# Optimization experiments

Measured on AMD Instinct MI355X. Metric: run time of the kernel, lower is better.

## Reference

```python
import jax, jax.numpy as jnp
import numpy as np

D = 1024
H = 16
T_BLOCK = 2048


def setup_inputs() -> dict:
    key = jax.random.key(0)
    ks = jax.random.split(key, 12)
    B, T = 2, 2048
    s = lambda k, shape: jax.random.normal(k, shape, jnp.float32) * 0.02
    return {
        "x": jax.random.normal(ks[0], (B, T, D), jnp.float32),
        # layernorms
        "ln1_g": jnp.ones((D,), jnp.float32), "ln1_b": jnp.zeros((D,), jnp.float32),
        "ln2_g": jnp.ones((D,), jnp.float32), "ln2_b": jnp.zeros((D,), jnp.float32),
        # attention qkv projection ([in,out] layout) and output proj
        "w_qkv": s(ks[1], (D, 3 * D)), "b_qkv": jnp.zeros((3 * D,), jnp.float32),
        "w_o": s(ks[2], (D, D)), "b_o": jnp.zeros((D,), jnp.float32),
        # MLP
        "w_fc1": s(ks[3], (D, 4 * D)), "b_fc1": jnp.zeros((4 * D,), jnp.float32),
        "w_fc2": s(ks[4], (4 * D, D)), "b_fc2": jnp.zeros((D,), jnp.float32),
    }


def _layernorm(x, g, b, eps=1e-5):
    mu = jnp.mean(x, axis=-1, keepdims=True)
    var = jnp.var(x, axis=-1, keepdims=True)
    return (x - mu) * jax.lax.rsqrt(var + eps) * g + b


def _attention(x, w_qkv, b_qkv, w_o, b_o):
    B, T, C = x.shape
    hd = C // H
    qkv = x @ w_qkv + b_qkv                      # [B,T,3C]
    q, k, v = jnp.split(qkv, 3, axis=-1)
    split = lambda t: t.reshape(B, T, H, hd).transpose(0, 2, 1, 3)  # [B,H,T,hd]
    q, k, v = split(q), split(k), split(v)
    att = jnp.einsum("bhqd,bhkd->bhqk", q, k) / jnp.sqrt(jnp.float32(hd))
    causal = jnp.tril(jnp.ones((T, T), bool))
    att = jnp.where(causal[None, None], att, -jnp.inf)
    att = jax.nn.softmax(att, axis=-1)
    y = jnp.einsum("bhqk,bhkd->bhqd", att, v)    # [B,H,T,hd]
    y = y.transpose(0, 2, 1, 3).reshape(B, T, C)
    return y @ w_o + b_o


def reference(x, ln1_g, ln1_b, ln2_g, ln2_b, w_qkv, b_qkv, w_o, b_o,
              w_fc1, b_fc1, w_fc2, b_fc2):
    # dropout is identity in eval mode
    x = x + _attention(_layernorm(x, ln1_g, ln1_b), w_qkv, b_qkv, w_o, b_o)
    h = jax.nn.gelu(_layernorm(x, ln2_g, ln2_b) @ w_fc1 + b_fc1)
    return x + (h @ w_fc2 + b_fc2)
```

## Files before the change

### kernel.cpp

```cpp
#include <hip/hip_runtime.h>
#include <hip/hip_bf16.h>


using bf16 = __bf16;
using bf16x8 = __attribute__((ext_vector_type(8))) __bf16;
using floatx4 = __attribute__((ext_vector_type(4))) float;

#define D_ 1024
#define T_ 2048
#define B_ 2
#define H_ 16

static __device__ __forceinline__ bf16 f2bf(float f) { return (bf16)f; }

static __device__ __forceinline__ void async16(const void* g, void* l) {
  __builtin_amdgcn_global_load_lds(
      (const __attribute__((address_space(1))) void*)g,
      (__attribute__((address_space(3))) void*)l, 16, 0, 0);
}

static __device__ __forceinline__ float gelu_f(float v) {
  const float u2 = 1.5957691216057308f * (v + 0.044715f * v * v * v);
  return v / (1.0f + __expf(-u2));
}

__global__ void transpose_cast(const float* __restrict__ in, bf16* __restrict__ out,
                               int K, int N) {
  __shared__ float tile[32][33];
  const int n0 = blockIdx.x * 32, k0 = blockIdx.y * 32;
  const int tx = threadIdx.x, ty = threadIdx.y;
  for (int i = 0; i < 32; i += 8)
    tile[ty + i][tx] = in[(size_t)(k0 + ty + i) * N + n0 + tx];
  __syncthreads();
  for (int i = 0; i < 32; i += 8)
    out[(size_t)(n0 + ty + i) * K + k0 + tx] = f2bf(tile[tx][ty + i]);
}

__global__ __launch_bounds__(256)
void ln_kernel(const float* __restrict__ x, const float* __restrict__ g,
               const float* __restrict__ bsh, bf16* __restrict__ out) {
  const int row = blockIdx.x, tid = threadIdx.x;
  const float4 v = ((const float4*)(x + (size_t)row * D_))[tid];
  float s = v.x + v.y + v.z + v.w;
  float s2 = v.x * v.x + v.y * v.y + v.z * v.z + v.w * v.w;
  for (int off = 32; off; off >>= 1) {
    s += __shfl_xor(s, off);
    s2 += __shfl_xor(s2, off);
  }
  __shared__ float red[8];
  const int wave = tid >> 6, lane = tid & 63;
  if (lane == 0) { red[wave] = s; red[wave + 4] = s2; }
  __syncthreads();
  s = red[0] + red[1] + red[2] + red[3];
  s2 = red[4] + red[5] + red[6] + red[7];
  const float mu = s * (1.0f / D_);
  const float rstd = rsqrtf(s2 * (1.0f / D_) - mu * mu + 1e-5f);
  const float4 gv = ((const float4*)g)[tid];
  const float4 bv = ((const float4*)bsh)[tid];
  bf16 o[4] __attribute__((aligned(8)));
  o[0] = f2bf((v.x - mu) * rstd * gv.x + bv.x);
  o[1] = f2bf((v.y - mu) * rstd * gv.y + bv.y);
  o[2] = f2bf((v.z - mu) * rstd * gv.z + bv.z);
  o[3] = f2bf((v.w - mu) * rstd * gv.w + bv.w);
  *(ushort4*)(out + (size_t)row * D_ + tid * 4) = *(const ushort4*)o;
}

template <int EPI>
__global__ __launch_bounds__(256)
void gemm_bt(const bf16* __restrict__ A, const bf16* __restrict__ Bt,
             const float* __restrict__ bias, const float* __restrict__ res,
             void* __restrict__ Cout, int M, int N, int K) {
  __shared__ __align__(16) bf16 As[128][64];
  __shared__ __align__(16) bf16 Bs[128][64];
  const int tid = threadIdx.x;
  const int wave = tid >> 6, lane = tid & 63;
  const int quad = lane >> 4, l16 = lane & 15;
  const int wr = wave >> 1, wc = wave & 1;
  const int bm = blockIdx.x * 128, bn = blockIdx.y * 128;
  const int lrow8 = lane >> 3;
  const int lcol = (((lane & 7) ^ lrow8) * 8);

  floatx4 acc[4][4] = {};

  for (int k0 = 0; k0 < K; k0 += 64) {
    __syncthreads();
    for (int c = 0; c < 4; c++) {
      const int r = wave * 32 + c * 8;
      async16(&A[(size_t)(bm + r + lrow8) * K + k0 + lcol], &As[r][0]);
      async16(&Bt[(size_t)(bn + r + lrow8) * K + k0 + lcol], &Bs[r][0]);
    }
    __syncthreads();
    for (int ks = 0; ks < 2; ks++) {
      const int fc = ((quad + ks * 4) ^ (l16 & 7)) * 8;
      bf16x8 af[4], bfr[4];
      for (int mt = 0; mt < 4; mt++)
        af[mt] = *(const bf16x8*)&As[wr * 64 + mt * 16 + l16][fc];
      for (int nt = 0; nt < 4; nt++)
        bfr[nt] = *(const bf16x8*)&Bs[wc * 64 + nt * 16 + l16][fc];
      for (int mt = 0; mt < 4; mt++)
        for (int nt = 0; nt < 4; nt++)
          acc[mt][nt] = __builtin_amdgcn_mfma_f32_16x16x32_bf16(
              af[mt], bfr[nt], acc[mt][nt], 0, 0, 0);
    }
  }

  for (int mt = 0; mt < 4; mt++) {
    for (int nt = 0; nt < 4; nt++) {
      const int col = bn + wc * 64 + nt * 16 + l16;
      const float bcol = bias[col];
      for (int i = 0; i < 4; i++) {
        const int row = bm + wr * 64 + mt * 16 + quad * 4 + i;
        float v = acc[mt][nt][i] + bcol;
        if (EPI == 0) {
          ((bf16*)Cout)[(size_t)row * N + col] = f2bf(v);
        } else if (EPI == 1) {
          ((bf16*)Cout)[(size_t)row * N + col] = f2bf(gelu_f(v));
        } else {
          ((float*)Cout)[(size_t)row * N + col] = v + res[(size_t)row * N + col];
        }
      }
    }
  }
}

template <int EPI>
__global__ __launch_bounds__(256)
void gemm64_k128(const bf16* __restrict__ A, const bf16* __restrict__ Bt,
                 const float* __restrict__ bias, const float* __restrict__ res,
                 void* __restrict__ Cout, int M, int N, int K) {
  __shared__ __align__(16) bf16 As[64][128];
  __shared__ __align__(16) bf16 Bs[128][128];
  const int tid = threadIdx.x;
  const int wave = tid >> 6, lane = tid & 63;
  const int quad = lane >> 4, l16 = lane & 15;
  const int wr = wave >> 1, wc = wave & 1;
  const int bm = blockIdx.x * 64, bn = blockIdx.y * 128;
  const int sr = lane >> 4;
  const int pchunk = lane & 15;

  floatx4 acc[2][4] = {};

  for (int k0 = 0; k0 < K; k0 += 128) {
    __syncthreads();
    for (int c = 0; c < 4; c++) {
      const int base = wave * 16 + c * 4;
      const int scol = (pchunk ^ ((c * 4 + sr) & 15)) * 8;
      async16(&A[(size_t)(bm + base + sr) * K + k0 + scol], &As[base][0]);
    }
    for (int c = 0; c < 8; c++) {
      const int base = wave * 32 + c * 4;
      const int scol = (pchunk ^ ((c * 4 + sr) & 15)) * 8;
      async16(&Bt[(size_t)(bn + base + sr) * K + k0 + scol], &Bs[base][0]);
    }
    __syncthreads();
    for (int ks = 0; ks < 4; ks++) {
      const int fc = ((quad + ks * 4) ^ l16) * 8;
      bf16x8 af[2], bfr[4];
      for (int mt = 0; mt < 2; mt++)
        af[mt] = *(const bf16x8*)&As[wr * 32 + mt * 16 + l16][fc];
      for (int nt = 0; nt < 4; nt++)
        bfr[nt] = *(const bf16x8*)&Bs[wc * 64 + nt * 16 + l16][fc];
      for (int mt = 0; mt < 2; mt++)
        for (int nt = 0; nt < 4; nt++)
          acc[mt][nt] = __builtin_amdgcn_mfma_f32_16x16x32_bf16(
              af[mt], bfr[nt], acc[mt][nt], 0, 0, 0);
    }
  }

  for (int mt = 0; mt < 2; mt++) {
    for (int nt = 0; nt < 4; nt++) {
      const int col = bn + wc * 64 + nt * 16 + l16;
      const float bcol = bias[col];
      for (int i = 0; i < 4; i++) {
        const int row = bm + wr * 32 + mt * 16 + quad * 4 + i;
        float v = acc[mt][nt][i] + bcol;
        if (EPI == 0) {
          ((bf16*)Cout)[(size_t)row * N + col] = f2bf(v);
        } else if (EPI == 1) {
          ((bf16*)Cout)[(size_t)row * N + col] = f2bf(gelu_f(v));
        } else {
          ((float*)Cout)[(size_t)row * N + col] = v + res[(size_t)row * N + col];
        }
      }
    }
  }
}

__global__ __launch_bounds__(512)
void attn_kernel(const bf16* __restrict__ qkv, bf16* __restrict__ y) {
  const int bh = blockIdx.y, b = bh >> 4, h = bh & 15;
  const int tile = (blockIdx.y & 16) ? (int)blockIdx.x : (15 - (int)blockIdx.x);
  const int q0 = tile * 128;
  const int tid = threadIdx.x, wave = tid >> 6, lane = tid & 63;
  const int quad = lane >> 4, l16 = lane & 15;
  const int l7 = l16 & 7;
  const int w16 = wave * 16;

  __shared__ __align__(16) bf16 Ks[64][64];
  __shared__ __align__(16) bf16 Vts[64][64];
  __shared__ __align__(16) bf16 Ps[128][64];

  const size_t bbase = (size_t)b * T_ * 3072 + (size_t)h * 64;
  const bf16* Qg = qkv + bbase;
  const bf16* Kg = qkv + bbase + 1024;
  const bf16* Vg = qkv + bbase + 2048;

  bf16x8 ones;
  for (int j = 0; j < 8; j++) ones[j] = f2bf(1.0f);

  const int kr = tid >> 3, kch = tid & 7;
  const int kcol = ((kch ^ (kr & 7)) * 8);
  const int vk = tid & 63, vd = tid >> 6;

  bf16x8 qf[2];
  for (int ks = 0; ks < 2; ks++) {
    bf16x8 t = *(const bf16x8*)
        &Qg[(size_t)(q0 + w16 + l16) * 3072 + ks * 32 + quad * 8];
    for (int j = 0; j < 8; j++) t[j] = f2bf((float)t[j] * 0.125f);
    qf[ks] = t;
  }

  int4 kreg = *(const int4*)&Kg[(size_t)kr * 3072 + kch * 8];
  bf16x8 vreg = *(const bf16x8*)&Vg[(size_t)vk * 3072 + vd * 8];

  floatx4 accY[4] = {};
  floatx4 accL = {};

  const int kend = q0 + 64;
  for (int kc = 0; kc <= kend; kc += 64) {
    __syncthreads();
    *(int4*)&Ks[kr][kcol] = kreg;
    for (int j = 0; j < 8; j++) {
      const int d = vd * 8 + j;
      Vts[d][((vk >> 3) ^ j) * 8 + (vk & 7)] = vreg[j];
    }
    __syncthreads();

    if (kc < kend) {
      kreg = *(const int4*)&Kg[(size_t)(kc + 64 + kr) * 3072 + kch * 8];
      vreg = *(const bf16x8*)&Vg[(size_t)(kc + 64 + vk) * 3072 + vd * 8];
    }

    floatx4 s[4];
    for (int nt = 0; nt < 4; nt++) {
      const bf16* krow = &Ks[nt * 16 + l16][0];
      bf16x8 kf0 = *(const bf16x8*)&krow[(quad ^ l7) * 8];
      bf16x8 kf1 = *(const bf16x8*)&krow[((4 + quad) ^ l7) * 8];
      floatx4 t = {};
      t = __builtin_amdgcn_mfma_f32_16x16x32_bf16(qf[0], kf0, t, 0, 0, 0);
      t = __builtin_amdgcn_mfma_f32_16x16x32_bf16(qf[1], kf1, t, 0, 0, 0);
      s[nt] = t;
    }
    if (kc + 64 > q0 + w16) {
      for (int nt = 0; nt < 4; nt++)
        for (int i = 0; i < 4; i++) {
          const int c = kc + nt * 16 + l16;
          const int r = q0 + w16 + quad * 4 + i;
          if (c > r) s[nt][i] = -1e30f;
        }
    }

    for (int i = 0; i < 4; i++) {
      const int pr = quad * 4 + i;
      bf16* prow = &Ps[w16 + pr][0];
      for (int nt = 0; nt < 4; nt++)
        prow[(((nt * 2 + (l16 >> 3)) ^ (pr & 7)) * 8) + l7] =
            f2bf(__expf(s[nt][i] - 8.0f));
    }
    __builtin_amdgcn_wave_barrier();

    for (int ks = 0; ks < 2; ks++) {
      bf16x8 pa = *(const bf16x8*)&Ps[w16 + l16][((ks * 4 + quad) ^ l7) * 8];
      for (int dt = 0; dt < 4; dt++) {
        bf16x8 vb = *(const bf16x8*)&Vts[dt * 16 + l16][((ks * 4 + quad) ^ l7) * 8];
        accY[dt] =
            __builtin_amdgcn_mfma_f32_16x16x32_bf16(pa, vb, accY[dt], 0, 0, 0);
      }
      accL = __builtin_amdgcn_mfma_f32_16x16x32_bf16(pa, ones, accL, 0, 0, 0);
    }
  }

  for (int i = 0; i < 4; i++) {
    const float linv = 1.0f / accL[i];
    const int r = q0 + w16 + quad * 4 + i;
    for (int dt = 0; dt < 4; dt++)
      y[(size_t)(b * T_ + r) * D_ + h * 64 + dt * 16 + l16] =
          f2bf(accY[dt][i] * linv);
  }
}

extern "C" void kernel_launch(void* const* d_in, const int* in_sizes, int n_in,
                              void* d_out, int out_size, void* d_ws, size_t ws_size,
                              hipStream_t stream) {
  const float* x     = (const float*)d_in[0];
  const float* ln1_g = (const float*)d_in[1];
  const float* ln1_b = (const float*)d_in[2];
  const float* ln2_g = (const float*)d_in[3];
  const float* ln2_b = (const float*)d_in[4];
  const float* w_qkv = (const float*)d_in[5];
  const float* b_qkv = (const float*)d_in[6];
  const float* w_o   = (const float*)d_in[7];
  const float* b_o   = (const float*)d_in[8];
  const float* w_fc1 = (const float*)d_in[9];
  const float* b_fc1 = (const float*)d_in[10];
  const float* w_fc2 = (const float*)d_in[11];
  const float* b_fc2 = (const float*)d_in[12];

  char* p = (char*)d_ws;
  bf16* wqkvT = (bf16*)p; p += (size_t)3072 * 1024 * 2;
  bf16* woT   = (bf16*)p; p += (size_t)1024 * 1024 * 2;
  bf16* wfc1T = (bf16*)p; p += (size_t)4096 * 1024 * 2;
  bf16* wfc2T = (bf16*)p; p += (size_t)1024 * 4096 * 2;
  bf16* ln1   = (bf16*)p; p += (size_t)4096 * 1024 * 2;
  bf16* qkv   = (bf16*)p; p += (size_t)4096 * 3072 * 2;
  bf16* yb    = (bf16*)p; p += (size_t)4096 * 1024 * 2;
  float* x2   = (float*)p; p += (size_t)4096 * 1024 * 4;
  bf16* ln2   = (bf16*)p; p += (size_t)4096 * 1024 * 2;
  bf16* hb    = (bf16*)p; p += (size_t)4096 * 4096 * 2;

  const dim3 tb(32, 8);
  transpose_cast<<<dim3(96, 32), tb, 0, stream>>>(w_qkv, wqkvT, 1024, 3072);
  transpose_cast<<<dim3(32, 32), tb, 0, stream>>>(w_o, woT, 1024, 1024);
  transpose_cast<<<dim3(128, 32), tb, 0, stream>>>(w_fc1, wfc1T, 1024, 4096);
  transpose_cast<<<dim3(32, 128), tb, 0, stream>>>(w_fc2, wfc2T, 4096, 1024);

  ln_kernel<<<4096, 256, 0, stream>>>(x, ln1_g, ln1_b, ln1);
  gemm_bt<0><<<dim3(32, 24), 256, 0, stream>>>(ln1, wqkvT, b_qkv, nullptr, qkv,
                                               4096, 3072, 1024);
  attn_kernel<<<dim3(16, 32), 512, 0, stream>>>(qkv, yb);
  gemm64_k128<2><<<dim3(64, 8), 256, 0, stream>>>(yb, woT, b_o, x, x2,
                                                  4096, 1024, 1024);
  ln_kernel<<<4096, 256, 0, stream>>>(x2, ln2_g, ln2_b, ln2);
  gemm_bt<1><<<dim3(32, 32), 256, 0, stream>>>(ln2, wfc1T, b_fc1, nullptr, hb,
                                               4096, 4096, 1024);
  gemm64_k128<2><<<dim3(64, 8), 256, 0, stream>>>(hb, wfc2T, b_fc2, x2, (float*)d_out,
                                                  4096, 1024, 4096);
}
```

Baseline: 319.0 us.

## Double-buffer LDS tiles in gemm_bt with async prefetch two steps ahead

Converts the 128x128 GEMM main loop to a two-stage LDS ping-pong. The global-to-LDS loads for step t+2 are issued while step t computes, and a partial vmcnt wait lets in-flight loads overlap MFMA work. This removes the full load-then-compute serialization of each K step, at the cost of doubling LDS use to 64KB per block, which may lower occupancy.

Measured after the change: 319.1 us. No clear change (+0.0%).

```diff
diff --git a/kernel.cpp b/kernel.cpp
--- a/kernel.cpp
+++ b/kernel.cpp
@@ -70,8 +70,8 @@
 void gemm_bt(const bf16* __restrict__ A, const bf16* __restrict__ Bt,
              const float* __restrict__ bias, const float* __restrict__ res,
              void* __restrict__ Cout, int M, int N, int K) {
-  __shared__ __align__(16) bf16 As[128][64];
-  __shared__ __align__(16) bf16 Bs[128][64];
+  __shared__ __align__(16) bf16 As[2][128][64];
+  __shared__ __align__(16) bf16 Bs[2][128][64];
   const int tid = threadIdx.x;
   const int wave = tid >> 6, lane = tid & 63;
   const int quad = lane >> 4, l16 = lane & 15;
@@ -80,37 +80,55 @@
   const int lrow8 = lane >> 3;
   const int lcol = (((lane & 7) ^ lrow8) * 8);
 
+  const bf16* aBase = &A[(size_t)(bm + wave * 32 + lrow8) * K + lcol];
+  const bf16* bBase = &Bt[(size_t)(bn + wave * 32 + lrow8) * K + lcol];
+
+  auto stage = [&](int buf, int kk) {
+    const int k0 = kk * 64;
+    for (int c = 0; c < 4; c++) {
+      async16(aBase + (size_t)c * 8 * K + k0, &As[buf][wave * 32 + c * 8][0]);
+      async16(bBase + (size_t)c * 8 * K + k0, &Bs[buf][wave * 32 + c * 8][0]);
+    }
+  };
+
   floatx4 acc[4][4] = {};
-
-  for (int k0 = 0; k0 < K; k0 += 64) {
-    __syncthreads();
-    for (int c = 0; c < 4; c++) {
-      const int r = wave * 32 + c * 8;
-      async16(&A[(size_t)(bm + r + lrow8) * K + k0 + lcol], &As[r][0]);
-      async16(&Bt[(size_t)(bn + r + lrow8) * K + k0 + lcol], &Bs[r][0]);
-    }
-    __syncthreads();
+  const int nsteps = K >> 6;
+
+  stage(0, 0);
+  if (nsteps > 1) stage(1, 1);
+  int cur = 0;
+  for (int t = 0; t < nsteps; ++t) {
+    if (t < nsteps - 1)
+      asm volatile("s_waitcnt vmcnt(8)" ::: "memory");
+    else
+      asm volatile("s_waitcnt vmcnt(0)" ::: "memory");
+    __builtin_amdgcn_s_barrier();
+    __builtin_amdgcn_sched_barrier(0);
     for (int ks = 0; ks < 2; ks++) {
       const int fc = ((quad + ks * 4) ^ (l16 & 7)) * 8;
       bf16x8 af[4], bfr[4];
       for (int mt = 0; mt < 4; mt++)
-        af[mt] = *(const bf16x8*)&As[wr * 64 + mt * 16 + l16][fc];
-      for (int nt = 0; nt < 4; nt++)
-        bfr[nt] = *(const bf16x8*)&Bs[wc * 64 + nt * 16 + l16][fc];
+        af[mt] = *(const bf16x8*)&As[cur][wr * 64 + mt * 16 + l16][fc];
+      for (int nn = 0; nn < 4; nn++)
+        bfr[nn] = *(const bf16x8*)&Bs[cur][wc * 64 + nn * 16 + l16][fc];
       for (int mt = 0; mt < 4; mt++)
-        for (int nt = 0; nt < 4; nt++)
-          acc[mt][nt] = __builtin_amdgcn_mfma_f32_16x16x32_bf16(
-              af[mt], bfr[nt], acc[mt][nt], 0, 0, 0);
-    }
+        for (int nn = 0; nn < 4; nn++)
+          acc[mt][nn] = __builtin_amdgcn_mfma_f32_16x16x32_bf16(
+              af[mt], bfr[nn], acc[mt][nn], 0, 0, 0);
+    }
+    __builtin_amdgcn_sched_barrier(0);
+    __builtin_amdgcn_s_barrier();
+    if (t + 2 < nsteps) stage(cur, t + 2);
+    cur ^= 1;
   }
 
   for (int mt = 0; mt < 4; mt++) {
-    for (int nt = 0; nt < 4; nt++) {
-      const int col = bn + wc * 64 + nt * 16 + l16;
+    for (int nn = 0; nn < 4; nn++) {
+      const int col = bn + wc * 64 + nn * 16 + l16;
       const float bcol = bias[col];
       for (int i = 0; i < 4; i++) {
         const int row = bm + wr * 64 + mt * 16 + quad * 4 + i;
-        float v = acc[mt][nt][i] + bcol;
+        float v = acc[mt][nn][i] + bcol;
         if (EPI == 0) {
           ((bf16*)Cout)[(size_t)row * N + col] = f2bf(v);
         } else if (EPI == 1) {
```
